# Optimization experiments

Hardware: AMD Instinct MI355X
Metric: run time of the kernel (lower is better)

Reference implementation:

```python
import jax, jax.numpy as jnp
import numpy as np

N = 20000          # num_nodes
R = 48             # num_relations
NB = 12            # num_bases
E = 640000         # num_edges (avg degree 32)
INIT, M1, M2 = 128, 128, 128
OUT3 = 512 - M2 - M1 - INIT  # = 128, per output_size arithmetic in __init__


def setup_inputs() -> dict:
    key = jax.random.key(0)
    ks = jax.random.split(key, 20)
    p = lambda k, shape, s=0.05: jax.random.normal(k, shape, jnp.float32) * s
    return {
        "emb": p(ks[0], (N, INIT)),
        "edge_src": jax.random.randint(ks[1], (E,), 0, N),
        "edge_dst": jax.random.randint(ks[2], (E,), 0, N),
        "edge_types": jax.random.randint(ks[3], (E,), 0, R),
        "comp1": p(ks[4], (R, NB), 0.3), "basis1": p(ks[5], (NB, INIT, M1)),
        "root1": p(ks[6], (INIT, M1)), "bias1": jnp.zeros((M1,), jnp.float32),
        "comp2": p(ks[7], (R, NB), 0.3), "basis2": p(ks[8], (NB, M1, M2)),
        "root2": p(ks[9], (M1, M2)), "bias2": jnp.zeros((M2,), jnp.float32),
        "comp3": p(ks[10], (R, NB), 0.3), "basis3": p(ks[11], (NB, M2, OUT3)),
        "root3": p(ks[12], (M2, OUT3)), "bias3": jnp.zeros((OUT3,), jnp.float32),
    }


def rgcn_conv(x, src, dst, etype, comp, basis, root, bias):
    """PyG RGCNConv with basis decomposition and per-relation mean aggregation.
    out_i = bias + x_i @ root + sum_r W_r^T . mean_{j in N_r(i)} x_j
    Mean aggregation commutes with the linear map, so aggregate raw features per
    (relation, target) first, then apply the relation weights as one batched GEMM.
    """
    Fin = x.shape[1]
    W = jnp.einsum('rb,bio->rio', comp, basis)                 # [R, Fin, Fout]
    seg = etype * N + dst                                      # fused (rel, dst) id
    msg = jax.ops.segment_sum(x[src], seg, num_segments=R * N) # [R*N, Fin]
    cnt = jax.ops.segment_sum(jnp.ones((src.shape[0], 1), x.dtype), seg,
                              num_segments=R * N)
    agg = (msg / jnp.maximum(cnt, 1.0)).reshape(R, N, Fin)     # mean, 0 if no edges
    return jnp.einsum('rni,rio->no', agg, W) + x @ root + bias


def reference(emb, edge_src, edge_dst, edge_types,
              comp1, basis1, root1, bias1,
              comp2, basis2, root2, bias2,
              comp3, basis3, root3, bias3):
    x1 = jax.nn.relu(rgcn_conv(emb, edge_src, edge_dst, edge_types,
                               comp1, basis1, root1, bias1))
    x2 = jax.nn.relu(rgcn_conv(x1, edge_src, edge_dst, edge_types,
                               comp2, basis2, root2, bias2))
    x3 = jax.nn.relu(rgcn_conv(x2, edge_src, edge_dst, edge_types,
                               comp3, basis3, root3, bias3))
    # dropout(0.2) is identity in eval mode
    return jnp.concatenate((x3, x2, x1, emb), axis=1)          # [N, 512]
```

## Files before the change

### kernel.cpp

```cpp
#include <hip/hip_runtime.h>
#include <hip/hip_bf16.h>

#define N_NODES 20000
#define R_REL   48
#define NBASES  12
#define E_EDGES 640000
#define KDIM    1664
#define KSTEPS  52
#define SLOTS   96
#define CPAD    8
#define PF      8

typedef __attribute__((ext_vector_type(8))) short bf16x8;
typedef __attribute__((ext_vector_type(4))) float f32x4;

__device__ inline float loadF(const void* p, long long idx, int isf32) {
    if (isf32 != 0) return ((const float*)p)[idx];
    return __bfloat162float(((const __hip_bfloat16*)p)[idx]);
}

__device__ inline void storeF(void* p, long long idx, int isf32, float v) {
    if (isf32 != 0) ((float*)p)[idx] = v;
    else ((__hip_bfloat16*)p)[idx] = __float2bfloat16(v);
}

__device__ inline unsigned short toBf(float v) {
    __hip_bfloat16 h = __float2bfloat16(v);
    return *(unsigned short*)&h;
}

__global__ void detect_dtype(const void* emb, int* flag) {
    if (threadIdx.x == 0 && blockIdx.x == 0) {
        const unsigned short* h = (const unsigned short*)emb;
        int f32 = 0;
        for (int k = 0; k < 256; k++) {
            unsigned int bits = ((unsigned int)h[k]) << 16;
            float v = __uint_as_float(bits);
            if (!(fabsf(v) < 1000.0f)) f32 = 1;
        }
        *flag = f32;
    }
}

__global__ void zero_i32(int* p, int n) {
    int i = blockIdx.x * 256 + threadIdx.x;
    if (i < n) p[i] = 0;
}

__global__ void scatter_d96(const int* src, const int* dst, const int* typ,
                            int* cursordP, int* s_pack) {
    int e = blockIdx.x * 256 + threadIdx.x;
    if (e < E_EDGES) {
        int d = dst[e];
        int pos = atomicAdd(&cursordP[d * CPAD], 1);
        if (pos < SLOTS)
            s_pack[d * SLOTS + pos] = src[e] | (typ[e] << 20);
    }
}

__global__ void build_wcat3(const void* b0, const void* r0,
                            const void* b1, const void* r1,
                            const void* b2, const void* r2,
                            __hip_bfloat16* Wt, const int* flagp) {
    int l = blockIdx.z;
    const void* basis = (l == 0) ? b0 : (l == 1) ? b1 : b2;
    const void* root  = (l == 0) ? r0 : (l == 1) ? r1 : r2;
    int o = blockIdx.x;
    int k = blockIdx.y * 256 + threadIdx.x;
    if (k >= KDIM) return;
    int isf32 = *flagp;
    float v;
    if (k < NBASES * 128) {
        int b = k >> 7, i = k & 127;
        v = loadF(basis, b * 16384 + i * 128 + o, isf32);
    } else {
        v = loadF(root, (k - NBASES * 128) * 128 + o, isf32);
    }
    Wt[(long long)l * (128 * KDIM) + (long long)o * KDIM + k] =
        __float2bfloat16(v);
}

__global__ void copy_emb_xc(const void* emb, void* out, float* xc,
                            const int* flagp) {
    int idx = blockIdx.x * 256 + threadIdx.x;
    int n = idx >> 4;
    int c8 = (idx & 15) * 8;
    float4 f0, f1;
    if (*flagp) {
        const float4* s = (const float4*)((const float*)emb +
                                          (long long)n * 128 + c8);
        f0 = s[0]; f1 = s[1];
        float4* d = (float4*)((float*)out + (long long)n * 512 + 384 + c8);
        d[0] = f0;
        d[1] = f1;
    } else {
        uint4 v = *(const uint4*)((const unsigned short*)emb +
                                  (long long)n * 128 + c8);
        *(uint4*)((unsigned short*)out + (long long)n * 512 + 384 + c8) = v;
        f0.x = __uint_as_float(v.x << 16);
        f0.y = __uint_as_float(v.x & 0xFFFF0000u);
        f0.z = __uint_as_float(v.y << 16);
        f0.w = __uint_as_float(v.y & 0xFFFF0000u);
        f1.x = __uint_as_float(v.z << 16);
        f1.y = __uint_as_float(v.z & 0xFFFF0000u);
        f1.z = __uint_as_float(v.w << 16);
        f1.w = __uint_as_float(v.w & 0xFFFF0000u);
    }
    float4* xd = (float4*)(xc + (long long)n * 128 + c8);
    xd[0] = f0;
    xd[1] = f1;
}

#define FX(j, idx) do {                                                       \
    int p_ = spkw[idx];                                                       \
    pp[j] = p_;                                                               \
    sx[j] = *(const float2*)(xc + (long long)(p_ & 0xFFFFF) * 128 + col);     \
} while (0)

#define CX(j) do {                                                            \
    int rel_ = pp[j] >> 20;                                                   \
    const float* cp_ = &scSw[rel_ * NBASES];                                  \
    float4 cA_ = *(const float4*)cp_;                                         \
    float4 cB_ = *(const float4*)(cp_ + 4);                                   \
    float4 cC_ = *(const float4*)(cp_ + 8);                                   \
    float x0_ = sx[j].x, x1_ = sx[j].y;                                       \
    accA[0]  += cA_.x * x0_;  accB[0]  += cA_.x * x1_;                        \
    accA[1]  += cA_.y * x0_;  accB[1]  += cA_.y * x1_;                        \
    accA[2]  += cA_.z * x0_;  accB[2]  += cA_.z * x1_;                        \
    accA[3]  += cA_.w * x0_;  accB[3]  += cA_.w * x1_;                        \
    accA[4]  += cB_.x * x0_;  accB[4]  += cB_.x * x1_;                        \
    accA[5]  += cB_.y * x0_;  accB[5]  += cB_.y * x1_;                        \
    accA[6]  += cB_.z * x0_;  accB[6]  += cB_.z * x1_;                        \
    accA[7]  += cB_.w * x0_;  accB[7]  += cB_.w * x1_;                        \
    accA[8]  += cC_.x * x0_;  accB[8]  += cC_.x * x1_;                        \
    accA[9]  += cC_.y * x0_;  accB[9]  += cC_.y * x1_;                        \
    accA[10] += cC_.z * x0_;  accB[10] += cC_.z * x1_;                        \
    accA[11] += cC_.w * x0_;  accB[11] += cC_.w * x1_;                        \
} while (0)

__global__ __launch_bounds__(256) void aggregate(
        const int* s_pack, const int* cntP, const void* comp,
        const float* xc, unsigned short* A, const int* flagp) {
    __shared__ float scomp[R_REL * NBASES];
    __shared__ float scS[4][R_REL * NBASES];
    __shared__ int   shcnt[4][R_REL];
    __shared__ int   spk[4][64];
    int isf32 = *flagp;
    int tid = threadIdx.x;
    int lane = tid & 63;
    int w = tid >> 6;
    int dstn = blockIdx.x * 4 + w;

    for (int i = tid; i < R_REL * NBASES; i += 256)
        scomp[i] = loadF(comp, i, isf32);
    __syncthreads();

    int cnt = cntP[dstn * CPAD]; if (cnt > SLOTS) cnt = SLOTS;
    int e0 = dstn * SLOTS;
    int e1 = e0 + cnt;
    int col = lane * 2;
    int* spkw = spk[w];
    float* scSw = scS[w];

    if (lane < R_REL) shcnt[w][lane] = 0;
    asm volatile("s_waitcnt lgkmcnt(0)" ::: "memory");
    for (int c0 = e0; c0 < e1; c0 += 64) {
        int e = c0 + lane;
        int p = s_pack[(e < e1) ? e : (e1 - 1)];
        if (c0 == e0) spkw[lane] = p;
        if (e < e1) atomicAdd(&shcnt[w][p >> 20], 1);
    }
    asm volatile("s_waitcnt lgkmcnt(0) vmcnt(0)" ::: "memory");
    if (lane < R_REL) {
        int c = shcnt[w][lane];
        float iv = (c > 0) ? (1.0f / (float)c) : 0.0f;
#pragma unroll
        for (int b = 0; b < NBASES; b++)
            scSw[lane * NBASES + b] = scomp[lane * NBASES + b] * iv;
    }
    asm volatile("s_waitcnt lgkmcnt(0)" ::: "memory");

    float accA[NBASES], accB[NBASES];
#pragma unroll
    for (int b = 0; b < NBASES; b++) { accA[b] = 0.0f; accB[b] = 0.0f; }

    for (int c0 = e0; c0 < e1; c0 += 64) {
        if (c0 != e0) {
            int e = c0 + lane;
            spkw[lane] = s_pack[(e < e1) ? e : (e1 - 1)];
        }
        asm volatile("s_waitcnt lgkmcnt(0)" ::: "memory");
        int cn = e1 - c0; if (cn > 64) cn = 64;
        float2 sx[PF]; int pp[PF];
#pragma unroll
        for (int j = 0; j < PF; j++)
            if (j < cn) FX(j, j);
        int i2 = 0;
        for (; i2 + PF <= cn; i2 += PF) {
#pragma unroll
            for (int j = 0; j < PF; j++) {
                CX(j);
                if (i2 + j + PF < cn) FX(j, i2 + j + PF);
            }
        }
#pragma unroll
        for (int j = 0; j < PF; j++)
            if (i2 + j < cn) CX(j);
    }

    unsigned short* Ar = A + (long long)dstn * KDIM;
#pragma unroll
    for (int b = 0; b < NBASES; b++) {
        unsigned int pk = ((unsigned int)toBf(accB[b]) << 16) |
                          (unsigned int)toBf(accA[b]);
        *(unsigned int*)(Ar + b * 128 + col) = pk;
    }
    {
        float2 f = *(const float2*)(xc + (long long)dstn * 128 + col);
        unsigned int pk = ((unsigned int)toBf(f.y) << 16) |
                          (unsigned int)toBf(f.x);
        *(unsigned int*)(Ar + NBASES * 128 + col) = pk;
    }
}

__global__ __launch_bounds__(256) void gemm_out(
        const __hip_bfloat16* A, const __hip_bfloat16* Wt,
        const void* bias, void* out, int slot,
        float* xc, int writeXc, const int* flagp) {
    int isf32 = *flagp;
    int tid = threadIdx.x;
    int lane = tid & 63;
    int w = tid >> 6;
    int lr = lane & 15;
    int lk = lane >> 4;
    int colBase = w * 32;
    int nb = blockIdx.x;
    const __hip_bfloat16* a0p = A + (long long)(nb * 32 + lr) * KDIM;
    const __hip_bfloat16* a1p = a0p + 16 * KDIM;
    const __hip_bfloat16* w0p = Wt + (long long)(colBase + lr) * KDIM;
    const __hip_bfloat16* w1p = w0p + 16 * KDIM;
    f32x4 acc00 = {0.f, 0.f, 0.f, 0.f};
    f32x4 acc01 = {0.f, 0.f, 0.f, 0.f};
    f32x4 acc10 = {0.f, 0.f, 0.f, 0.f};
    f32x4 acc11 = {0.f, 0.f, 0.f, 0.f};
#pragma unroll 4
    for (int ks = 0; ks < KSTEPS; ks++) {
        int ko = ks * 32 + lk * 8;
        bf16x8 a0 = *(const bf16x8*)(a0p + ko);
        bf16x8 a1 = *(const bf16x8*)(a1p + ko);
        bf16x8 b0 = *(const bf16x8*)(w0p + ko);
        bf16x8 b1 = *(const bf16x8*)(w1p + ko);
        acc00 = __builtin_amdgcn_mfma_f32_16x16x32_bf16(a0, b0, acc00, 0, 0, 0);
        acc01 = __builtin_amdgcn_mfma_f32_16x16x32_bf16(a0, b1, acc01, 0, 0, 0);
        acc10 = __builtin_amdgcn_mfma_f32_16x16x32_bf16(a1, b0, acc10, 0, 0, 0);
        acc11 = __builtin_amdgcn_mfma_f32_16x16x32_bf16(a1, b1, acc11, 0, 0, 0);
    }
    float bi0 = loadF(bias, colBase + lr, isf32);
    float bi1 = loadF(bias, colBase + 16 + lr, isf32);
#pragma unroll
    for (int q = 0; q < 4; q++) {
        int row = lk * 4 + q;
        int r0 = nb * 32 + row;
        int r1 = r0 + 16;
        float v00 = fmaxf(acc00[q] + bi0, 0.0f);
        float v01 = fmaxf(acc01[q] + bi1, 0.0f);
        float v10 = fmaxf(acc10[q] + bi0, 0.0f);
        float v11 = fmaxf(acc11[q] + bi1, 0.0f);
        long long n0 = (long long)r0 * 512 + slot;
        long long n1 = (long long)r1 * 512 + slot;
        storeF(out, n0 + colBase + lr,      isf32, v00);
        storeF(out, n0 + colBase + 16 + lr, isf32, v01);
        storeF(out, n1 + colBase + lr,      isf32, v10);
        storeF(out, n1 + colBase + 16 + lr, isf32, v11);
        if (writeXc) {
            xc[(long long)r0 * 128 + colBase + lr]      = v00;
            xc[(long long)r0 * 128 + colBase + 16 + lr] = v01;
            xc[(long long)r1 * 128 + colBase + lr]      = v10;
            xc[(long long)r1 * 128 + colBase + 16 + lr] = v11;
        }
    }
}

extern "C" void kernel_launch(void* const* d_in, const int* in_sizes, int n_in,
                              void* d_out, int out_size, void* d_ws, size_t ws_size,
                              hipStream_t stream) {
    const void* emb  = d_in[0];
    const int* esrc = (const int*)d_in[1];
    const int* edst = (const int*)d_in[2];
    const int* etyp = (const int*)d_in[3];
    const void* comp[3];
    const void* basis[3];
    const void* root[3];
    const void* bias[3];
    for (int l = 0; l < 3; l++) {
        comp[l]  = d_in[4 + l * 4];
        basis[l] = d_in[5 + l * 4];
        root[l]  = d_in[6 + l * 4];
        bias[l]  = d_in[7 + l * 4];
    }

    char* ws = (char*)d_ws;
    int*   flag     = (int*)(ws + 0);
    int*   s_pack   = (int*)(ws + 256);
    int*   cursordP = (int*)(ws + 7680256);
    __hip_bfloat16* Wt = (__hip_bfloat16*)(ws + 8320256);
    float* xc       = (float*)(ws + 9598208);
    unsigned short* A = (unsigned short*)(ws + 19838208);

    detect_dtype<<<1, 64, 0, stream>>>(emb, flag);
    zero_i32<<<625, 256, 0, stream>>>(cursordP, N_NODES * CPAD);
    scatter_d96<<<2500, 256, 0, stream>>>(esrc, edst, etyp, cursordP, s_pack);
    copy_emb_xc<<<1250, 256, 0, stream>>>(emb, d_out, xc, flag);
    build_wcat3<<<dim3(128, 7, 3), 256, 0, stream>>>(
        basis[0], root[0], basis[1], root[1], basis[2], root[2], Wt, flag);

    const int slots[3] = {256, 128, 0};
    for (int l = 0; l < 3; l++) {
        const __hip_bfloat16* Wtl = Wt + (long long)l * (128 * KDIM);
        aggregate<<<5000, 256, 0, stream>>>(s_pack, cursordP, comp[l],
                                            xc, A, flag);
        gemm_out<<<625, 256, 0, stream>>>((const __hip_bfloat16*)A, Wtl,
                                          bias[l], d_out, slots[l],
                                          xc, (l < 2) ? 1 : 0, flag);
    }
    (void)in_sizes; (void)n_in; (void)out_size; (void)ws_size;
}
```

Before: 600.4 us.

## Precompute per-relation inverse counts once and halve gemm row tile

Per-(node, relation) edge counts are accumulated with float atomics during the edge scatter and turned into reciprocals once. Each of the three aggregate launches then reads them instead of re-scanning its edge list with LDS atomics. Separately, the output GEMM tile drops from 32 to 16 rows per block, doubling the grid to 1250 blocks for more parallelism. The cost is 640k extra global atomics, one extra kernel, a larger zeroing pass, and lower per-block reuse of the weight loads in the GEMM.

```diff
diff --git a/kernel.cpp b/kernel.cpp
--- a/kernel.cpp
+++ b/kernel.cpp
@@ -48,14 +48,22 @@
 }
 
 __global__ void scatter_d96(const int* src, const int* dst, const int* typ,
-                            int* cursordP, int* s_pack) {
+                            int* cursordP, int* s_pack, float* cnt48) {
     int e = blockIdx.x * 256 + threadIdx.x;
     if (e < E_EDGES) {
         int d = dst[e];
+        int t = typ[e];
         int pos = atomicAdd(&cursordP[d * CPAD], 1);
         if (pos < SLOTS)
-            s_pack[d * SLOTS + pos] = src[e] | (typ[e] << 20);
-    }
+            s_pack[d * SLOTS + pos] = src[e] | (t << 20);
+        atomicAdd(&cnt48[d * R_REL + t], 1.0f);
+    }
+}
+
+__global__ void inv48_kernel(float* p) {
+    int i = blockIdx.x * 256 + threadIdx.x;
+    float c = p[i];
+    p[i] = (c > 0.0f) ? (1.0f / c) : 0.0f;
 }
 
 __global__ void build_wcat3(const void* b0, const void* r0,
@@ -139,11 +147,11 @@
 } while (0)
 
 __global__ __launch_bounds__(256) void aggregate(
-        const int* s_pack, const int* cntP, const void* comp,
-        const float* xc, unsigned short* A, const int* flagp) {
+        const int* s_pack, const int* cntP, const float* inv48,
+        const void* comp, const float* xc, unsigned short* A,
+        const int* flagp) {
     __shared__ float scomp[R_REL * NBASES];
     __shared__ float scS[4][R_REL * NBASES];
-    __shared__ int   shcnt[4][R_REL];
     __shared__ int   spk[4][64];
     int isf32 = *flagp;
     int tid = threadIdx.x;
@@ -162,30 +170,20 @@
     int* spkw = spk[w];
     float* scSw = scS[w];
 
-    if (lane < R_REL) shcnt[w][lane] = 0;
-    asm volatile("s_waitcnt lgkmcnt(0)" ::: "memory");
-    for (int c0 = e0; c0 < e1; c0 += 64) {
-        int e = c0 + lane;
-        int p = s_pack[(e < e1) ? e : (e1 - 1)];
-        if (c0 == e0) spkw[lane] = p;
-        if (e < e1) atomicAdd(&shcnt[w][p >> 20], 1);
-    }
-    asm volatile("s_waitcnt lgkmcnt(0) vmcnt(0)" ::: "memory");
     if (lane < R_REL) {
-        int c = shcnt[w][lane];
-        float iv = (c > 0) ? (1.0f / (float)c) : 0.0f;
+        float iv = inv48[dstn * R_REL + lane];
 #pragma unroll
         for (int b = 0; b < NBASES; b++)
             scSw[lane * NBASES + b] = scomp[lane * NBASES + b] * iv;
     }
-    asm volatile("s_waitcnt lgkmcnt(0)" ::: "memory");
+    asm volatile("s_waitcnt lgkmcnt(0) vmcnt(0)" ::: "memory");
 
     float accA[NBASES], accB[NBASES];
 #pragma unroll
     for (int b = 0; b < NBASES; b++) { accA[b] = 0.0f; accB[b] = 0.0f; }
 
     for (int c0 = e0; c0 < e1; c0 += 64) {
-        if (c0 != e0) {
+        {
             int e = c0 + lane;
             spkw[lane] = s_pack[(e < e1) ? e : (e1 - 1)];
         }
@@ -235,48 +233,34 @@
     int lk = lane >> 4;
     int colBase = w * 32;
     int nb = blockIdx.x;
-    const __hip_bfloat16* a0p = A + (long long)(nb * 32 + lr) * KDIM;
-    const __hip_bfloat16* a1p = a0p + 16 * KDIM;
+    const __hip_bfloat16* a0p = A + (long long)(nb * 16 + lr) * KDIM;
     const __hip_bfloat16* w0p = Wt + (long long)(colBase + lr) * KDIM;
     const __hip_bfloat16* w1p = w0p + 16 * KDIM;
-    f32x4 acc00 = {0.f, 0.f, 0.f, 0.f};
-    f32x4 acc01 = {0.f, 0.f, 0.f, 0.f};
-    f32x4 acc10 = {0.f, 0.f, 0.f, 0.f};
-    f32x4 acc11 = {0.f, 0.f, 0.f, 0.f};
+    f32x4 acc0 = {0.f, 0.f, 0.f, 0.f};
+    f32x4 acc1 = {0.f, 0.f, 0.f, 0.f};
 #pragma unroll 4
     for (int ks = 0; ks < KSTEPS; ks++) {
         int ko = ks * 32 + lk * 8;
         bf16x8 a0 = *(const bf16x8*)(a0p + ko);
-        bf16x8 a1 = *(const bf16x8*)(a1p + ko);
         bf16x8 b0 = *(const bf16x8*)(w0p + ko);
         bf16x8 b1 = *(const bf16x8*)(w1p + ko);
-        acc00 = __builtin_amdgcn_mfma_f32_16x16x32_bf16(a0, b0, acc00, 0, 0, 0);
-        acc01 = __builtin_amdgcn_mfma_f32_16x16x32_bf16(a0, b1, acc01, 0, 0, 0);
-        acc10 = __builtin_amdgcn_mfma_f32_16x16x32_bf16(a1, b0, acc10, 0, 0, 0);
-        acc11 = __builtin_amdgcn_mfma_f32_16x16x32_bf16(a1, b1, acc11, 0, 0, 0);
+        acc0 = __builtin_amdgcn_mfma_f32_16x16x32_bf16(a0, b0, acc0, 0, 0, 0);
+        acc1 = __builtin_amdgcn_mfma_f32_16x16x32_bf16(a0, b1, acc1, 0, 0, 0);
     }
     float bi0 = loadF(bias, colBase + lr, isf32);
     float bi1 = loadF(bias, colBase + 16 + lr, isf32);
 #pragma unroll
     for (int q = 0; q < 4; q++) {
         int row = lk * 4 + q;
-        int r0 = nb * 32 + row;
-        int r1 = r0 + 16;
-        float v00 = fmaxf(acc00[q] + bi0, 0.0f);
-        float v01 = fmaxf(acc01[q] + bi1, 0.0f);
-        float v10 = fmaxf(acc10[q] + bi0, 0.0f);
-        float v11 = fmaxf(acc11[q] + bi1, 0.0f);
+        int r0 = nb * 16 + row;
+        float v0 = fmaxf(acc0[q] + bi0, 0.0f);
+        float v1 = fmaxf(acc1[q] + bi1, 0.0f);
         long long n0 = (long long)r0 * 512 + slot;
-        long long n1 = (long long)r1 * 512 + slot;
-        storeF(out, n0 + colBase + lr,      isf32, v00);
-        storeF(out, n0 + colBase + 16 + lr, isf32, v01);
-        storeF(out, n1 + colBase + lr,      isf32, v10);
-        storeF(out, n1 + colBase + 16 + lr, isf32, v11);
+        storeF(out, n0 + colBase + lr,      isf32, v0);
+        storeF(out, n0 + colBase + 16 + lr, isf32, v1);
         if (writeXc) {
-            xc[(long long)r0 * 128 + colBase + lr]      = v00;
-            xc[(long long)r0 * 128 + colBase + 16 + lr] = v01;
-            xc[(long long)r1 * 128 + colBase + lr]      = v10;
-            xc[(long long)r1 * 128 + colBase + 16 + lr] = v11;
+            xc[(long long)r0 * 128 + colBase + lr]      = v0;
+            xc[(long long)r0 * 128 + colBase + 16 + lr] = v1;
         }
     }
 }
@@ -303,13 +287,16 @@
     int*   flag     = (int*)(ws + 0);
     int*   s_pack   = (int*)(ws + 256);
     int*   cursordP = (int*)(ws + 7680256);
-    __hip_bfloat16* Wt = (__hip_bfloat16*)(ws + 8320256);
-    float* xc       = (float*)(ws + 9598208);
-    unsigned short* A = (unsigned short*)(ws + 19838208);
+    float* cnt48    = (float*)(ws + 8320256);
+    __hip_bfloat16* Wt = (__hip_bfloat16*)(ws + 12160256);
+    float* xc       = (float*)(ws + 13438208);
+    unsigned short* A = (unsigned short*)(ws + 23678208);
 
     detect_dtype<<<1, 64, 0, stream>>>(emb, flag);
-    zero_i32<<<625, 256, 0, stream>>>(cursordP, N_NODES * CPAD);
-    scatter_d96<<<2500, 256, 0, stream>>>(esrc, edst, etyp, cursordP, s_pack);
+    zero_i32<<<4375, 256, 0, stream>>>(cursordP, N_NODES * CPAD + N_NODES * R_REL);
+    scatter_d96<<<2500, 256, 0, stream>>>(esrc, edst, etyp, cursordP,
+                                          s_pack, cnt48);
+    inv48_kernel<<<3750, 256, 0, stream>>>(cnt48);
     copy_emb_xc<<<1250, 256, 0, stream>>>(emb, d_out, xc, flag);
     build_wcat3<<<dim3(128, 7, 3), 256, 0, stream>>>(
         basis[0], root[0], basis[1], root[1], basis[2], root[2], Wt, flag);
@@ -317,11 +304,11 @@
     const int slots[3] = {256, 128, 0};
     for (int l = 0; l < 3; l++) {
         const __hip_bfloat16* Wtl = Wt + (long long)l * (128 * KDIM);
-        aggregate<<<5000, 256, 0, stream>>>(s_pack, cursordP, comp[l],
+        aggregate<<<5000, 256, 0, stream>>>(s_pack, cursordP, cnt48, comp[l],
                                             xc, A, flag);
-        gemm_out<<<625, 256, 0, stream>>>((const __hip_bfloat16*)A, Wtl,
-                                          bias[l], d_out, slots[l],
-                                          xc, (l < 2) ? 1 : 0, flag);
+        gemm_out<<<1250, 256, 0, stream>>>((const __hip_bfloat16*)A, Wtl,
+                                           bias[l], d_out, slots[l],
+                                           xc, (l < 2) ? 1 : 0, flag);
     }
     (void)in_sizes; (void)n_in; (void)out_size; (void)ws_size;
 }
```

Measured after the change: 674.9 us. 12.4% more time.
